# Performance work log

Measured on AMD Instinct MI355X. Metric: run time of the kernel, lower is better.

Reference implementation:

```python
import jax, jax.numpy as jnp
import numpy as np

# Model dims
P_SPECS = [(6, 256), (7, 256)]          # pattern_length -> num_patterns (ordered)
P = 512                                  # total_num_patterns
MAXL = 7                                 # max_pattern_length
ND = 2                                   # num_diags (self-loop diag + main diag)
D = 300                                  # embedding_dim
V = 50000                                # vocab size
B = 32                                   # batch size
T = 128                                  # max_doc_len
NC = 2                                   # num_classes
NEG = -1e30                              # max-sum semiring zero; one = 0.0
END_STATES = np.concatenate([np.full(n, l - 1, dtype=np.int32) for l, n in P_SPECS])


def setup_inputs() -> dict:
    key = jax.random.key(0)
    ks = jax.random.split(key, 8)
    tokens = jax.random.randint(ks[0], (B, T), 0, V, dtype=jnp.int32)
    doc_lens = jax.random.randint(ks[1], (B,), 64, T + 1, dtype=jnp.int32)
    emb_table = jax.random.normal(ks[2], (V, D), dtype=jnp.float32)
    diags = jax.random.normal(ks[3], (P * ND * MAXL, D), dtype=jnp.float32)
    diags = diags / jnp.linalg.norm(diags, axis=1, keepdims=True)  # normalize(diags)
    bias = jax.random.normal(ks[4], (P * ND * MAXL, 1), dtype=jnp.float32)
    epsilons = jax.random.normal(ks[5], (P, MAXL - 1), dtype=jnp.float32)
    bn_weight = jnp.ones((P,), jnp.float32)
    bn_bias = jnp.zeros((P,), jnp.float32)
    final_w = 0.05 * jax.random.normal(ks[6], (NC, P), dtype=jnp.float32)
    final_b = jnp.zeros((NC,), jnp.float32)
    return dict(tokens=tokens, doc_lens=doc_lens, emb_table=emb_table, diags=diags,
                bias=bias, epsilons=epsilons, bn_weight=bn_weight, bn_bias=bn_bias,
                final_w=final_w, final_b=final_b)


def reference(tokens, doc_lens, emb_table, diags, bias, epsilons,
              bn_weight, bn_bias, final_w, final_b):
    # --- transition matrices (max-sum semiring: from_outer is identity) ---
    emb = emb_table[tokens]                                   # [B,T,D]
    # mm(diags, embeddings) + bias_scale * bias  (bias_scale = 1.0)
    ts = jnp.einsum('btd,kd->btk', emb, diags) + bias[:, 0]   # [B,T,P*ND*MAXL]
    ts = ts.reshape(B, T, P, ND, MAXL)                        # [B,T,P,ND,MAXL]

    end = jnp.asarray(END_STATES)                             # [P]
    hid0 = jnp.full((B, P, MAXL), NEG, jnp.float32).at[:, :, 0].set(0.0)
    sc0 = jnp.full((B, P), NEG, jnp.float32)                  # semiring.zero
    zpad = jnp.full((B, P, 1), NEG, jnp.float32)              # zero_padding
    rpad = jnp.zeros((B, P, 1), jnp.float32)                  # restart_padding (one)

    # epsilon_values = epsilon_scale (one=0) + epsilons
    def step(carry, xs):
        hid, sc = carry
        tm, i = xs                                            # tm: [B,P,ND,MAXL]
        # epsilon transitions
        ae = jnp.maximum(hid, jnp.concatenate([zpad, hid[:, :, :-1] + epsilons], axis=2))
        # main path: diag index -1 (the main diagonal)
        main = jnp.concatenate([rpad, ae[:, :, :-1] + tm[:, :, -1, :-1]], axis=2)
        # self loops: diag 0, self_loop_scale = semiring.one = 0
        sl = ae + tm[:, :, 0, :]
        hid = jnp.maximum(main, sl)
        endv = jnp.take_along_axis(hid, jnp.broadcast_to(end[None, :, None], (B, P, 1)), axis=2)[:, :, 0]
        sc = jnp.where((doc_lens > i)[:, None], jnp.maximum(sc, endv), sc)
        return (hid, sc), None

    (_, scores), _ = jax.lax.scan(step, (hid0, sc0),
                                  (jnp.moveaxis(ts, 1, 0), jnp.arange(T, dtype=jnp.int32)))

    # BatchNorm1d (training mode: biased batch statistics)
    mean = scores.mean(axis=0)
    var = scores.var(axis=0)
    scores = (scores - mean) * jax.lax.rsqrt(var + 1e-5) * bn_weight + bn_bias
    # binarize_scores
    scores = jnp.sign(jax.nn.relu(scores))
    # final linear layer
    return scores @ final_w.T + final_b                       # [B, NC]
```

## Files before the change

kernel.cpp:

```cpp
#include <hip/hip_runtime.h>

#define BB 32
#define TT 128
#define PP 512
#define DD 300
#define KP 320
#define NR 13
#define NN 6656
#define NS 7168
#define NEG -1e30f

typedef _Float16 half8 __attribute__((ext_vector_type(8)));
typedef _Float16 half4 __attribute__((ext_vector_type(4)));
typedef float floatx4 __attribute__((ext_vector_type(4)));

__device__ __forceinline__ void async_load16(const void* g, void* l) {
    __builtin_amdgcn_global_load_lds(
        (const __attribute__((address_space(1))) void*)g,
        (__attribute__((address_space(3))) void*)l, 16, 0, 0);
}

__device__ __forceinline__ floatx4 mfma16(half8 a, half8 b, floatx4 c) {
    return __builtin_amdgcn_mfma_f32_16x16x32_f16(a, b, c, 0, 0, 0);
}

__global__ __launch_bounds__(256) void pack_kernel(
    const int* __restrict__ tokens, const float* __restrict__ emb,
    const float* __restrict__ diags, const float* __restrict__ bias,
    _Float16* __restrict__ Ah, _Float16* __restrict__ Al,
    _Float16* __restrict__ Bh, _Float16* __restrict__ Bl)
{
    const int idx = blockIdx.x * 256 + threadIdx.x;
    if (idx >= (4096 + NN) * 80) return;
    const int r = idx / 80;
    const int c = idx - r * 80;

    float4 x = make_float4(0.f, 0.f, 0.f, 0.f);
    _Float16* dh;
    _Float16* dl;

    if (r < 4096) {
        if (c < 75) x = *(const float4*)(emb + (size_t)tokens[r] * DD + c * 4);
        else if (c == 75) x.x = 1.0f;
        dh = Ah + (size_t)r * KP + c * 4;
        dl = Al + (size_t)r * KP + c * 4;
    } else {
        const int n = r - 4096;
        const int p = n / NR;
        const int rr = n - p * NR;
        const int srow = p * 14 + rr;
        if (c < 75) x = *(const float4*)(diags + (size_t)srow * DD + c * 4);
        else if (c == 75) x.x = bias[srow];
        dh = Bh + (size_t)n * KP + c * 4;
        dl = Bl + (size_t)n * KP + c * 4;
    }

    half4 h, l;
    h.x = (_Float16)x.x; l.x = (_Float16)((x.x - (float)h.x) * 4096.f);
    h.y = (_Float16)x.y; l.y = (_Float16)((x.y - (float)h.y) * 4096.f);
    h.z = (_Float16)x.z; l.z = (_Float16)((x.z - (float)h.z) * 4096.f);
    h.w = (_Float16)x.w; l.w = (_Float16)((x.w - (float)h.w) * 4096.f);
    if (r < 4096 && c == 75) { l.x = (_Float16)0.f; }
    *(half4*)dh = h;
    *(half4*)dl = l;
}

__global__ __launch_bounds__(256, 2) void gemm_kernel(
    const _Float16* __restrict__ Ah, const _Float16* __restrict__ Al,
    const _Float16* __restrict__ Bh, const _Float16* __restrict__ Bl,
    float* __restrict__ C)
{
    __shared__ __align__(16) _Float16 AsH[2][128 * 32];
    __shared__ __align__(16) _Float16 AsL[2][128 * 32];
    __shared__ __align__(16) _Float16 BsH[2][128 * 32];
    __shared__ __align__(16) _Float16 BsL[2][128 * 32];

    const int tid = threadIdx.x;
    const int w = tid >> 6, ln = tid & 63;
    const int n0 = blockIdx.x * 128, m0 = blockIdx.y * 128;
    const int wm = w & 1, wn = w >> 1;

    floatx4 acc0[4][4], acc1[4][4];
    #pragma unroll
    for (int i = 0; i < 4; ++i)
        #pragma unroll
        for (int j = 0; j < 4; ++j) {
            acc0[i][j] = (floatx4){0.f, 0.f, 0.f, 0.f};
            acc1[i][j] = (floatx4){0.f, 0.f, 0.f, 0.f};
        }

    const int srow = ln >> 2;
    const int sch  = (ln & 3) * 8;
    const int fr = ln & 15;
    const int kg = ln >> 4;

    const _Float16* gsrc = (w == 0) ? Ah + (size_t)m0 * KP
                        : (w == 1) ? Al + (size_t)m0 * KP
                        : (w == 2) ? Bh + (size_t)n0 * KP
                                   : Bl + (size_t)n0 * KP;
    _Float16* lbase = (w == 0) ? &AsH[0][0]
                    : (w == 1) ? &AsL[0][0]
                    : (w == 2) ? &BsH[0][0]
                               : &BsL[0][0];

    for (int kt = 0; kt < KP / 64; ++kt) {
        const int k0 = kt * 64;
        #pragma unroll
        for (int kb = 0; kb < 2; ++kb) {
            #pragma unroll
            for (int s = 0; s < 8; ++s) {
                async_load16(gsrc + (size_t)(s * 16 + srow) * KP + k0 + kb * 32 + sch,
                             lbase + kb * (128 * 32) + s * 16 * 32);
            }
        }
        __syncthreads();

        #pragma unroll
        for (int kb = 0; kb < 2; ++kb) {
            half8 ah4[4], al4[4];
            #pragma unroll
            for (int i = 0; i < 4; ++i) {
                const int off = (wm * 64 + i * 16 + fr) * 32 + kg * 8;
                ah4[i] = *(const half8*)&AsH[kb][off];
                al4[i] = *(const half8*)&AsL[kb][off];
            }
            #pragma unroll
            for (int j = 0; j < 4; ++j) {
                const int off = (wn * 64 + j * 16 + fr) * 32 + kg * 8;
                const half8 bh = *(const half8*)&BsH[kb][off];
                const half8 bl = *(const half8*)&BsL[kb][off];
                #pragma unroll
                for (int i = 0; i < 4; ++i) {
                    acc0[i][j] = mfma16(ah4[i], bh, acc0[i][j]);
                    acc1[i][j] = mfma16(ah4[i], bl, acc1[i][j]);
                    acc1[i][j] = mfma16(al4[i], bh, acc1[i][j]);
                }
            }
        }
        __syncthreads();
    }

    #pragma unroll
    for (int j = 0; j < 4; ++j) {
        const int n = n0 + wn * 64 + j * 16 + fr;
        const int col = n + (unsigned)n / 13u;
        #pragma unroll
        for (int i = 0; i < 4; ++i) {
            const int mb = m0 + wm * 64 + i * 16 + kg * 4;
            #pragma unroll
            for (int r = 0; r < 4; ++r)
                C[(size_t)(mb + r) * NS + col] =
                    acc0[i][j][r] + acc1[i][j][r] * (1.0f / 4096.0f);
        }
    }
}

__global__ __launch_bounds__(64) void scan_kernel(
    const float* __restrict__ ts,
    const float* __restrict__ epsilons,
    const int* __restrict__ doc_lens,
    float* __restrict__ scores)
{
    const int b = blockIdx.x;
    const int p = blockIdx.y * 64 + threadIdx.x;
    const int dl = doc_lens[b];

    float e[6];
    #pragma unroll
    for (int i = 0; i < 6; ++i) e[i] = epsilons[p * 6 + i];

    const float* base = ts + (size_t)b * TT * NS + p * 14;

    float h0 = 0.f, h1 = NEG, h2 = NEG, h3 = NEG, h4 = NEG, h5 = NEG, h6 = NEG;
    float sc = NEG;
    const bool end5 = (p < 256);

    float2 buf[4][7];

    auto load = [&](int slot, int t) {
        const float2* s = (const float2*)(base + (size_t)t * NS);
        #pragma unroll
        for (int i = 0; i < 7; ++i) buf[slot][i] = s[i];
    };
    auto step = [&](int slot, int t) {
        const float2* v = buf[slot];
        float ae0 = h0;
        float ae1 = fmaxf(h1, h0 + e[0]);
        float ae2 = fmaxf(h2, h1 + e[1]);
        float ae3 = fmaxf(h3, h2 + e[2]);
        float ae4 = fmaxf(h4, h3 + e[3]);
        float ae5 = fmaxf(h5, h4 + e[4]);
        float ae6 = fmaxf(h6, h5 + e[5]);
        h0 = fmaxf(0.f,            ae0 + v[0].x);
        h1 = fmaxf(ae0 + v[3].y,   ae1 + v[0].y);
        h2 = fmaxf(ae1 + v[4].x,   ae2 + v[1].x);
        h3 = fmaxf(ae2 + v[4].y,   ae3 + v[1].y);
        h4 = fmaxf(ae3 + v[5].x,   ae4 + v[2].x);
        h5 = fmaxf(ae4 + v[5].y,   ae5 + v[2].y);
        h6 = fmaxf(ae5 + v[6].x,   ae6 + v[3].x);
        const float endv = end5 ? h5 : h6;
        if (t < dl) sc = fmaxf(sc, endv);
    };

    #pragma unroll
    for (int j = 0; j < 4; ++j) load(j, j);

    for (int tb = 0; tb < TT - 4; tb += 4) {
        #pragma unroll
        for (int j = 0; j < 4; ++j) {
            step(j, tb + j);
            load(j, tb + j + 4);
        }
    }
    #pragma unroll
    for (int j = 0; j < 4; ++j) step(j, TT - 4 + j);

    scores[p * BB + b] = sc;
}

__global__ __launch_bounds__(512) void finalize_kernel(
    const float* __restrict__ scores,
    const float* __restrict__ bn_w,
    const float* __restrict__ bn_b,
    const float* __restrict__ fw,
    const float* __restrict__ fb,
    float* __restrict__ out)
{
    __shared__ float acc[64];
    const int p = threadIdx.x;
    if (p < 64) acc[p] = 0.f;
    __syncthreads();

    float x[32];
    const float4* sp = (const float4*)(scores + p * 32);
    #pragma unroll
    for (int i = 0; i < 8; ++i) ((float4*)x)[i] = sp[i];

    float mean = 0.f;
    #pragma unroll
    for (int i = 0; i < 32; ++i) mean += x[i];
    mean *= (1.f / 32.f);
    float var = 0.f;
    #pragma unroll
    for (int i = 0; i < 32; ++i) { const float d = x[i] - mean; var = fmaf(d, d, var); }
    var *= (1.f / 32.f);

    const float scale = (1.f / sqrtf(var + 1e-5f)) * bn_w[p];
    const float shift = bn_b[p];
    const float w0 = fw[p], w1 = fw[PP + p];

    for (int b = 0; b < 32; ++b) {
        const float v = (x[b] - mean) * scale + shift;
        const bool bin = v > 0.f;
        float v0 = bin ? w0 : 0.f;
        float v1 = bin ? w1 : 0.f;
        #pragma unroll
        for (int o = 32; o; o >>= 1) {
            v0 += __shfl_xor(v0, o);
            v1 += __shfl_xor(v1, o);
        }
        if ((threadIdx.x & 63) == 0) {
            atomicAdd(&acc[b * 2 + 0], v0);
            atomicAdd(&acc[b * 2 + 1], v1);
        }
    }
    __syncthreads();
    if (p < 64) out[p] = acc[p] + fb[p & 1];
}

extern "C" void kernel_launch(void* const* d_in, const int* in_sizes, int n_in,
                              void* d_out, int out_size, void* d_ws, size_t ws_size,
                              hipStream_t stream) {
    const int*   tokens   = (const int*)d_in[0];
    const int*   doc_lens = (const int*)d_in[1];
    const float* emb      = (const float*)d_in[2];
    const float* diags    = (const float*)d_in[3];
    const float* bias     = (const float*)d_in[4];
    const float* eps      = (const float*)d_in[5];
    const float* bnw      = (const float*)d_in[6];
    const float* bnb      = (const float*)d_in[7];
    const float* fw       = (const float*)d_in[8];
    const float* fb       = (const float*)d_in[9];
    float* out = (float*)d_out;

    float* ts     = (float*)d_ws;
    float* scores = ts + (size_t)4096 * NS;
    _Float16* Ah  = (_Float16*)(scores + PP * BB);
    _Float16* Al  = Ah + (size_t)4096 * KP;
    _Float16* Bh  = Al + (size_t)4096 * KP;
    _Float16* Bl  = Bh + (size_t)NN * KP;

    pack_kernel<<<((4096 + NN) * 80 + 255) / 256, 256, 0, stream>>>(
        tokens, emb, diags, bias, Ah, Al, Bh, Bl);
    gemm_kernel<<<dim3(NN / 128, 32), 256, 0, stream>>>(Ah, Al, Bh, Bl, ts);
    scan_kernel<<<dim3(32, 8), 64, 0, stream>>>(ts, eps, doc_lens, scores);
    finalize_kernel<<<1, 512, 0, stream>>>(scores, bnw, bnb, fw, fb, out);
}
```

Measured before the change: 223.5 us.

## Pre-pack operands in MFMA fragment order and transpose transition scores

The pack kernel now writes A and B in per-16-row, per-32-k fragment order, so the GEMM reads A fragments straight from global memory into registers and stages only B through LDS with a software double buffer. The GEMM writes the output transposed (n-major, m contiguous) as float4 stores, dropping the padded NS column layout. The scan then reads 13 float4 streams per pattern, each covering four timesteps, instead of 7 float2 per timestep. This aims to cut LDS traffic and sync in the GEMM and to make the scan's loads coalesced and wider, at the cost of more register pressure and uncoalesced direct-to-register A loads.

```diff
diff --git a/kernel.cpp b/kernel.cpp
--- a/kernel.cpp
+++ b/kernel.cpp
@@ -4,14 +4,14 @@
 #define TT 128
 #define PP 512
 #define DD 300
-#define KP 320
+#define KT 10
 #define NR 13
 #define NN 6656
-#define NS 7168
+#define AT 256
+#define BT 416
 #define NEG -1e30f
 
 typedef _Float16 half8 __attribute__((ext_vector_type(8)));
-typedef _Float16 half4 __attribute__((ext_vector_type(4)));
 typedef float floatx4 __attribute__((ext_vector_type(4)));
 
 __device__ __forceinline__ void async_load16(const void* g, void* l) {
@@ -27,57 +27,71 @@
 __global__ __launch_bounds__(256) void pack_kernel(
     const int* __restrict__ tokens, const float* __restrict__ emb,
     const float* __restrict__ diags, const float* __restrict__ bias,
-    _Float16* __restrict__ Ah, _Float16* __restrict__ Al,
-    _Float16* __restrict__ Bh, _Float16* __restrict__ Bl)
+    _Float16* __restrict__ AhP, _Float16* __restrict__ AlP,
+    _Float16* __restrict__ BhP, _Float16* __restrict__ BlP)
 {
     const int idx = blockIdx.x * 256 + threadIdx.x;
-    if (idx >= (4096 + NN) * 80) return;
-    const int r = idx / 80;
-    const int c = idx - r * 80;
-
-    float4 x = make_float4(0.f, 0.f, 0.f, 0.f);
-    _Float16* dh;
-    _Float16* dl;
-
-    if (r < 4096) {
-        if (c < 75) x = *(const float4*)(emb + (size_t)tokens[r] * DD + c * 4);
-        else if (c == 75) x.x = 1.0f;
-        dh = Ah + (size_t)r * KP + c * 4;
-        dl = Al + (size_t)r * KP + c * 4;
+    if (idx >= (AT + BT) * KT * 64) return;
+    const int chunk = idx >> 6;
+    const int ln = idx & 63;
+
+    const float* src;
+    float kslot;
+    _Float16 *dh, *dl;
+    int kt;
+    if (chunk < AT * KT) {
+        const int mt = chunk / KT; kt = chunk - mt * KT;
+        const int m = mt * 16 + (ln & 15);
+        src = emb + (size_t)tokens[m] * DD;
+        kslot = 1.0f;
+        dh = AhP + (size_t)chunk * 512 + ln * 8;
+        dl = AlP + (size_t)chunk * 512 + ln * 8;
     } else {
-        const int n = r - 4096;
+        const int c2 = chunk - AT * KT;
+        const int nt = c2 / KT; kt = c2 - nt * KT;
+        const int n = nt * 16 + (ln & 15);
         const int p = n / NR;
-        const int rr = n - p * NR;
-        const int srow = p * 14 + rr;
-        if (c < 75) x = *(const float4*)(diags + (size_t)srow * DD + c * 4);
-        else if (c == 75) x.x = bias[srow];
-        dh = Bh + (size_t)n * KP + c * 4;
-        dl = Bl + (size_t)n * KP + c * 4;
-    }
-
-    half4 h, l;
-    h.x = (_Float16)x.x; l.x = (_Float16)((x.x - (float)h.x) * 4096.f);
-    h.y = (_Float16)x.y; l.y = (_Float16)((x.y - (float)h.y) * 4096.f);
-    h.z = (_Float16)x.z; l.z = (_Float16)((x.z - (float)h.z) * 4096.f);
-    h.w = (_Float16)x.w; l.w = (_Float16)((x.w - (float)h.w) * 4096.f);
-    if (r < 4096 && c == 75) { l.x = (_Float16)0.f; }
-    *(half4*)dh = h;
-    *(half4*)dl = l;
+        const int srow = p * 14 + (n - p * NR);
+        src = diags + (size_t)srow * DD;
+        kslot = bias[srow];
+        dh = BhP + (size_t)c2 * 512 + ln * 8;
+        dl = BlP + (size_t)c2 * 512 + ln * 8;
+    }
+
+    const int k0 = kt * 32 + (ln >> 4) * 8;
+    float v[8];
+    if (k0 + 8 <= DD) {
+        float4 a = *(const float4*)(src + k0);
+        float4 b = *(const float4*)(src + k0 + 4);
+        v[0] = a.x; v[1] = a.y; v[2] = a.z; v[3] = a.w;
+        v[4] = b.x; v[5] = b.y; v[6] = b.z; v[7] = b.w;
+    } else {
+        #pragma unroll
+        for (int i = 0; i < 8; ++i) {
+            const int k = k0 + i;
+            v[i] = (k < DD) ? src[k] : (k == DD ? kslot : 0.f);
+        }
+    }
+    half8 h, l;
+    #pragma unroll
+    for (int i = 0; i < 8; ++i) {
+        h[i] = (_Float16)v[i];
+        l[i] = (_Float16)((v[i] - (float)h[i]) * 4096.f);
+    }
+    *(half8*)dh = h;
+    *(half8*)dl = l;
 }
 
 __global__ __launch_bounds__(256, 2) void gemm_kernel(
-    const _Float16* __restrict__ Ah, const _Float16* __restrict__ Al,
-    const _Float16* __restrict__ Bh, const _Float16* __restrict__ Bl,
+    const _Float16* __restrict__ AhP, const _Float16* __restrict__ AlP,
+    const _Float16* __restrict__ BhP, const _Float16* __restrict__ BlP,
     float* __restrict__ C)
 {
-    __shared__ __align__(16) _Float16 AsH[2][128 * 32];
-    __shared__ __align__(16) _Float16 AsL[2][128 * 32];
-    __shared__ __align__(16) _Float16 BsH[2][128 * 32];
-    __shared__ __align__(16) _Float16 BsL[2][128 * 32];
+    __shared__ __align__(16) _Float16 Bs[2][2][8][512];
 
     const int tid = threadIdx.x;
     const int w = tid >> 6, ln = tid & 63;
-    const int n0 = blockIdx.x * 128, m0 = blockIdx.y * 128;
+    const int n0t = blockIdx.x * 8, m0t = blockIdx.y * 8;
     const int wm = w & 1, wn = w >> 1;
 
     floatx4 acc0[4][4], acc1[4][4];
@@ -89,74 +103,69 @@
             acc1[i][j] = (floatx4){0.f, 0.f, 0.f, 0.f};
         }
 
-    const int srow = ln >> 2;
-    const int sch  = (ln & 3) * 8;
-    const int fr = ln & 15;
-    const int kg = ln >> 4;
-
-    const _Float16* gsrc = (w == 0) ? Ah + (size_t)m0 * KP
-                        : (w == 1) ? Al + (size_t)m0 * KP
-                        : (w == 2) ? Bh + (size_t)n0 * KP
-                                   : Bl + (size_t)n0 * KP;
-    _Float16* lbase = (w == 0) ? &AsH[0][0]
-                    : (w == 1) ? &AsL[0][0]
-                    : (w == 2) ? &BsH[0][0]
-                               : &BsL[0][0];
-
-    for (int kt = 0; kt < KP / 64; ++kt) {
-        const int k0 = kt * 64;
-        #pragma unroll
-        for (int kb = 0; kb < 2; ++kb) {
-            #pragma unroll
-            for (int s = 0; s < 8; ++s) {
-                async_load16(gsrc + (size_t)(s * 16 + srow) * KP + k0 + kb * 32 + sch,
-                             lbase + kb * (128 * 32) + s * 16 * 32);
-            }
-        }
-        __syncthreads();
-
-        #pragma unroll
-        for (int kb = 0; kb < 2; ++kb) {
-            half8 ah4[4], al4[4];
+    half8 ah[2][4], al[2][4];
+
+    auto loadA = [&](int kt, int pb) {
+        #pragma unroll
+        for (int i = 0; i < 4; ++i) {
+            const size_t ch = ((size_t)(m0t + wm * 4 + i) * KT + kt) * 512 + ln * 8;
+            ah[pb][i] = *(const half8*)(AhP + ch);
+            al[pb][i] = *(const half8*)(AlP + ch);
+        }
+    };
+    auto stageB = [&](int kt, int buf) {
+        #pragma unroll
+        for (int s = 0; s < 2; ++s) {
+            const int nt = w + s * 4;
+            const size_t ch = ((size_t)(n0t + nt) * KT + kt) * 512 + ln * 8;
+            async_load16(BhP + ch, &Bs[buf][0][nt][0]);
+            async_load16(BlP + ch, &Bs[buf][1][nt][0]);
+        }
+    };
+
+    stageB(0, 0);
+    loadA(0, 0);
+    __syncthreads();
+
+    #pragma unroll
+    for (int kt = 0; kt < KT; ++kt) {
+        const int cb = kt & 1, nb = cb ^ 1;
+        if (kt + 1 < KT) {
+            loadA(kt + 1, nb);
+            stageB(kt + 1, nb);
+        }
+        #pragma unroll
+        for (int j = 0; j < 4; ++j) {
+            const half8 bh = *(const half8*)&Bs[cb][0][wn * 4 + j][ln * 8];
+            const half8 bl = *(const half8*)&Bs[cb][1][wn * 4 + j][ln * 8];
             #pragma unroll
             for (int i = 0; i < 4; ++i) {
-                const int off = (wm * 64 + i * 16 + fr) * 32 + kg * 8;
-                ah4[i] = *(const half8*)&AsH[kb][off];
-                al4[i] = *(const half8*)&AsL[kb][off];
+                acc0[i][j] = mfma16(ah[cb][i], bh, acc0[i][j]);
+                acc1[i][j] = mfma16(ah[cb][i], bl, acc1[i][j]);
+                acc1[i][j] = mfma16(al[cb][i], bh, acc1[i][j]);
             }
-            #pragma unroll
-            for (int j = 0; j < 4; ++j) {
-                const int off = (wn * 64 + j * 16 + fr) * 32 + kg * 8;
-                const half8 bh = *(const half8*)&BsH[kb][off];
-                const half8 bl = *(const half8*)&BsL[kb][off];
-                #pragma unroll
-                for (int i = 0; i < 4; ++i) {
-                    acc0[i][j] = mfma16(ah4[i], bh, acc0[i][j]);
-                    acc1[i][j] = mfma16(ah4[i], bl, acc1[i][j]);
-                    acc1[i][j] = mfma16(al4[i], bh, acc1[i][j]);
-                }
-            }
         }
         __syncthreads();
     }
 
     #pragma unroll
     for (int j = 0; j < 4; ++j) {
-        const int n = n0 + wn * 64 + j * 16 + fr;
-        const int col = n + (unsigned)n / 13u;
+        const int n = (n0t + wn * 4 + j) * 16 + (ln & 15);
         #pragma unroll
         for (int i = 0; i < 4; ++i) {
-            const int mb = m0 + wm * 64 + i * 16 + kg * 4;
-            #pragma unroll
-            for (int r = 0; r < 4; ++r)
-                C[(size_t)(mb + r) * NS + col] =
-                    acc0[i][j][r] + acc1[i][j][r] * (1.0f / 4096.0f);
-        }
-    }
-}
-
-__global__ __launch_bounds__(64) void scan_kernel(
-    const float* __restrict__ ts,
+            const int m = (m0t + wm * 4 + i) * 16 + (ln >> 4) * 4;
+            float4 v;
+            v.x = acc0[i][j][0] + acc1[i][j][0] * (1.0f / 4096.0f);
+            v.y = acc0[i][j][1] + acc1[i][j][1] * (1.0f / 4096.0f);
+            v.z = acc0[i][j][2] + acc1[i][j][2] * (1.0f / 4096.0f);
+            v.w = acc0[i][j][3] + acc1[i][j][3] * (1.0f / 4096.0f);
+            *(float4*)(C + (size_t)n * 4096 + m) = v;
+        }
+    }
+}
+
+__global__ __launch_bounds__(64, 1) void scan_kernel(
+    const float* __restrict__ tsT,
     const float* __restrict__ epsilons,
     const int* __restrict__ doc_lens,
     float* __restrict__ scores)
@@ -169,51 +178,50 @@
     #pragma unroll
     for (int i = 0; i < 6; ++i) e[i] = epsilons[p * 6 + i];
 
-    const float* base = ts + (size_t)b * TT * NS + p * 14;
+    const float* base = tsT + (size_t)p * NR * 4096 + b * TT;
 
     float h0 = 0.f, h1 = NEG, h2 = NEG, h3 = NEG, h4 = NEG, h5 = NEG, h6 = NEG;
     float sc = NEG;
     const bool end5 = (p < 256);
 
-    float2 buf[4][7];
-
-    auto load = [&](int slot, int t) {
-        const float2* s = (const float2*)(base + (size_t)t * NS);
-        #pragma unroll
-        for (int i = 0; i < 7; ++i) buf[slot][i] = s[i];
+    float4 buf[3][NR];
+
+    auto load = [&](int slot, int q) {
+        #pragma unroll
+        for (int s = 0; s < NR; ++s)
+            buf[slot][s] = *(const float4*)(base + (size_t)s * 4096 + q * 4);
     };
-    auto step = [&](int slot, int t) {
-        const float2* v = buf[slot];
-        float ae0 = h0;
-        float ae1 = fmaxf(h1, h0 + e[0]);
-        float ae2 = fmaxf(h2, h1 + e[1]);
-        float ae3 = fmaxf(h3, h2 + e[2]);
-        float ae4 = fmaxf(h4, h3 + e[3]);
-        float ae5 = fmaxf(h5, h4 + e[4]);
-        float ae6 = fmaxf(h6, h5 + e[5]);
-        h0 = fmaxf(0.f,            ae0 + v[0].x);
-        h1 = fmaxf(ae0 + v[3].y,   ae1 + v[0].y);
-        h2 = fmaxf(ae1 + v[4].x,   ae2 + v[1].x);
-        h3 = fmaxf(ae2 + v[4].y,   ae3 + v[1].y);
-        h4 = fmaxf(ae3 + v[5].x,   ae4 + v[2].x);
-        h5 = fmaxf(ae4 + v[5].y,   ae5 + v[2].y);
-        h6 = fmaxf(ae5 + v[6].x,   ae6 + v[3].x);
-        const float endv = end5 ? h5 : h6;
-        if (t < dl) sc = fmaxf(sc, endv);
-    };
-
-    #pragma unroll
-    for (int j = 0; j < 4; ++j) load(j, j);
-
-    for (int tb = 0; tb < TT - 4; tb += 4) {
-        #pragma unroll
-        for (int j = 0; j < 4; ++j) {
-            step(j, tb + j);
-            load(j, tb + j + 4);
-        }
-    }
-    #pragma unroll
-    for (int j = 0; j < 4; ++j) step(j, TT - 4 + j);
+
+    #define STEPC(slot, comp, t) do {                                        \
+        float ae0 = h0;                                                       \
+        float ae1 = fmaxf(h1, h0 + e[0]);                                     \
+        float ae2 = fmaxf(h2, h1 + e[1]);                                     \
+        float ae3 = fmaxf(h3, h2 + e[2]);                                     \
+        float ae4 = fmaxf(h4, h3 + e[3]);                                     \
+        float ae5 = fmaxf(h5, h4 + e[4]);                                     \
+        float ae6 = fmaxf(h6, h5 + e[5]);                                     \
+        h0 = fmaxf(0.f,                       ae0 + buf[slot][0].comp);       \
+        h1 = fmaxf(ae0 + buf[slot][7].comp,   ae1 + buf[slot][1].comp);       \
+        h2 = fmaxf(ae1 + buf[slot][8].comp,   ae2 + buf[slot][2].comp);       \
+        h3 = fmaxf(ae2 + buf[slot][9].comp,   ae3 + buf[slot][3].comp);       \
+        h4 = fmaxf(ae3 + buf[slot][10].comp,  ae4 + buf[slot][4].comp);       \
+        h5 = fmaxf(ae4 + buf[slot][11].comp,  ae5 + buf[slot][5].comp);       \
+        h6 = fmaxf(ae5 + buf[slot][12].comp,  ae6 + buf[slot][6].comp);       \
+        const float endv = end5 ? h5 : h6;                                    \
+        if ((t) < dl) sc = fmaxf(sc, endv); } while (0)
+
+    load(0, 0); load(1, 1); load(2, 2);
+    #pragma unroll
+    for (int q = 0; q < 32; ++q) {
+        const int slot = q % 3;
+        const int t0 = q * 4;
+        STEPC(slot, x, t0 + 0);
+        STEPC(slot, y, t0 + 1);
+        STEPC(slot, z, t0 + 2);
+        STEPC(slot, w, t0 + 3);
+        if (q + 3 < 32) load(slot, q + 3);
+    }
+    #undef STEPC
 
     scores[p * BB + b] = sc;
 }
@@ -283,16 +291,16 @@
     const float* fb       = (const float*)d_in[9];
     float* out = (float*)d_out;
 
-    float* ts     = (float*)d_ws;
-    float* scores = ts + (size_t)4096 * NS;
-    _Float16* Ah  = (_Float16*)(scores + PP * BB);
-    _Float16* Al  = Ah + (size_t)4096 * KP;
-    _Float16* Bh  = Al + (size_t)4096 * KP;
-    _Float16* Bl  = Bh + (size_t)NN * KP;
-
-    pack_kernel<<<((4096 + NN) * 80 + 255) / 256, 256, 0, stream>>>(
-        tokens, emb, diags, bias, Ah, Al, Bh, Bl);
-    gemm_kernel<<<dim3(NN / 128, 32), 256, 0, stream>>>(Ah, Al, Bh, Bl, ts);
-    scan_kernel<<<dim3(32, 8), 64, 0, stream>>>(ts, eps, doc_lens, scores);
+    float* tsT    = (float*)d_ws;
+    float* scores = tsT + (size_t)NN * 4096;
+    _Float16* AhP = (_Float16*)(scores + PP * BB);
+    _Float16* AlP = AhP + (size_t)AT * KT * 512;
+    _Float16* BhP = AlP + (size_t)AT * KT * 512;
+    _Float16* BlP = BhP + (size_t)BT * KT * 512;
+
+    pack_kernel<<<(AT + BT) * KT * 64 / 256, 256, 0, stream>>>(
+        tokens, emb, diags, bias, AhP, AlP, BhP, BlP);
+    gemm_kernel<<<dim3(BT / 8, AT / 8), 256, 0, stream>>>(AhP, AlP, BhP, BlP, tsT);
+    scan_kernel<<<dim3(BB, 8), 64, 0, stream>>>(tsT, eps, doc_lens, scores);
     finalize_kernel<<<1, 512, 0, stream>>>(scores, bnw, bnb, fw, fb, out);
 }
```

New measurement: 264.4 us. 1.18x slower.
